# Kernel tuning notes

Measured on AMD Instinct MI355X. Metric: run time of the kernel, lower is better.

Reference implementation:

```python
import jax, jax.numpy as jnp
import numpy as np

BN_EPS = 1e-5

def conv1x1(x, w, b):
    # x: [B,C,H,W], w: [O,C], b: [O] -> [B,O,H,W]
    return jnp.einsum('bchw,oc->bohw', x, w) + b[None, :, None, None]

def maxpool2x2(x):
    B, C, H, W = x.shape
    return x.reshape(B, C, H // 2, 2, W // 2, 2).max(axis=(3, 5))

def setup_inputs() -> dict:
    key = jax.random.key(0)
    ks = jax.random.split(key, 12)
    B, C, Ci, H, W = 8, 256, 128, 64, 64
    s_in = 1.0 / np.sqrt(C)
    s_mid = 1.0 / np.sqrt(Ci)
    return {
        'x': jax.random.normal(ks[0], (B, C, H, W), jnp.float32),
        'y': jax.random.normal(ks[1], (B, C, H, W), jnp.float32),
        'theta_w': jax.random.normal(ks[2], (Ci, C), jnp.float32) * s_in,
        'theta_b': jax.random.normal(ks[3], (Ci,), jnp.float32) * s_in,
        'phi_w': jax.random.normal(ks[4], (Ci, C), jnp.float32) * s_in,
        'phi_b': jax.random.normal(ks[5], (Ci,), jnp.float32) * s_in,
        'g_w': jax.random.normal(ks[6], (Ci, C), jnp.float32) * s_in,
        'g_b': jax.random.normal(ks[7], (Ci,), jnp.float32) * s_in,
        'w_w': jax.random.normal(ks[8], (C, Ci), jnp.float32) * s_mid,
        'w_b': jax.random.normal(ks[9], (C,), jnp.float32) * s_mid,
        'bn_gamma': jax.random.normal(ks[10], (C,), jnp.float32),
        'bn_beta': jax.random.normal(ks[11], (C,), jnp.float32),
    }

def reference(x, y, theta_w, theta_b, phi_w, phi_b, g_w, g_b, w_w, w_b, bn_gamma, bn_beta):
    B, C, H, W = x.shape
    Ci = theta_w.shape[0]
    # Q: [B, N, Ci] from x (no subsample)
    theta_x = conv1x1(x, theta_w, theta_b).reshape(B, Ci, H * W).transpose(0, 2, 1)
    # K: [B, Ci, M] and V: [B, M, Ci] from y (2x2 maxpool subsample)
    phi_x = maxpool2x2(conv1x1(y, phi_w, phi_b)).reshape(B, Ci, -1)
    g_x = maxpool2x2(conv1x1(y, g_w, g_b)).reshape(B, Ci, -1).transpose(0, 2, 1)
    # unscaled dot-product attention, softmax over keys
    f = jnp.einsum('bnc,bcm->bnm', theta_x, phi_x)        # [B, N, M]
    attn = jax.nn.softmax(f, axis=-1)
    out = jnp.einsum('bnm,bmc->bnc', attn, g_x)            # [B, N, Ci]
    out = out.transpose(0, 2, 1).reshape(B, Ci, H, W)
    # W projection (1x1 conv) + BatchNorm (batch statistics, training mode)
    wy = conv1x1(out, w_w, w_b)
    mean = wy.mean(axis=(0, 2, 3))
    var = wy.var(axis=(0, 2, 3))
    wy = (wy - mean[None, :, None, None]) * jax.lax.rsqrt(var[None, :, None, None] + BN_EPS)
    wy = wy * bn_gamma[None, :, None, None] + bn_beta[None, :, None, None]
    return wy + x
```

## Files before the change

kernel.cpp:

```cpp
#include <hip/hip_runtime.h>

#define B_  8
#define C_  256
#define CI_ 128
#define N_  4096
#define M_  1024

typedef unsigned short u16;
typedef _Float16 f16;
typedef __attribute__((ext_vector_type(8))) short short8;
typedef __attribute__((ext_vector_type(8))) _Float16 half8;
typedef __attribute__((ext_vector_type(4))) _Float16 half4;
typedef __attribute__((ext_vector_type(4))) float f32x4;

__device__ __forceinline__ u16 f2bf(float f) {
    unsigned int u = __float_as_uint(f);
    u += 0x7fffu + ((u >> 16) & 1u);
    return (u16)(u >> 16);
}

__global__ __launch_bounds__(256) void prep_w_kernel(
    const float* __restrict__ tw, const float* __restrict__ pw,
    const float* __restrict__ gw, const float* __restrict__ ww,
    f16* __restrict__ out_h)
{
    int t = blockIdx.x * 256 + threadIdx.x;
    int wsel = t >> 12, idx = t & 4095;
    int lane = idx & 63;
    const float* src; int F, Cdim;
    if (wsel == 3)      { src = ww; F = 16; Cdim = 128; }
    else if (wsel == 0) { src = tw; F = 8;  Cdim = 256; }
    else if (wsel == 1) { src = pw; F = 8;  Cdim = 256; }
    else                { src = gw; F = 8;  Cdim = 256; }
    int fk = idx >> 6;
    int ks = fk / F, f = fk - ks * F;
    int o = f * 16 + (lane & 15);
    int c = ks * 32 + (lane >> 4) * 8;
    const float* s = src + (size_t)o * Cdim + c;
    float4 v0 = *(const float4*)s;
    float4 v1 = *(const float4*)(s + 4);
    half8 hv;
    hv[0] = (f16)v0.x; hv[1] = (f16)v0.y; hv[2] = (f16)v0.z; hv[3] = (f16)v0.w;
    hv[4] = (f16)v1.x; hv[5] = (f16)v1.y; hv[6] = (f16)v1.z; hv[7] = (f16)v1.w;
    size_t oo = (size_t)wsel * 32768 + (size_t)idx * 8;
    *(half8*)&out_h[oo] = hv;
}

__global__ __launch_bounds__(256) void qconv_kernel(
    const float* __restrict__ x,
    const f16* __restrict__ Bfh, const float* __restrict__ bias,
    f16* __restrict__ qh_out)
{
    const int tid = threadIdx.x;
    const int wave = tid >> 6, lane = tid & 63;
    const int tx = lane & 15, quad = lane >> 4;
    const int id = blockIdx.x;
    const int ot = (id >> 3) & 1;
    const int p  = (id & 7) | ((id >> 4) << 3);
    const int nb = p & 63;
    const int b  = p >> 6;
    const int nw = nb * 64 + wave * 16;

    f32x4 acc[4];
    #pragma unroll
    for (int i = 0; i < 4; ++i) acc[i] = (f32x4){0.f, 0.f, 0.f, 0.f};

    #pragma unroll
    for (int ks = 0; ks < 8; ++ks) {
        const size_t cbase = ((size_t)b * C_ + ks * 32 + quad * 8) * N_ + nw + tx;
        float a[8];
        #pragma unroll
        for (int j = 0; j < 8; ++j) a[j] = x[cbase + (size_t)j * N_];
        half8 ah;
        #pragma unroll
        for (int j = 0; j < 8; ++j) ah[j] = (f16)a[j];
        #pragma unroll
        for (int fi = 0; fi < 4; ++fi) {
            int f = ot * 4 + fi;
            size_t bo = ((size_t)(ks * 8 + f) * 64 + lane) * 8;
            half8 bh = *(const half8*)&Bfh[bo];
            acc[fi] = __builtin_amdgcn_mfma_f32_16x16x32_f16(ah, bh, acc[fi], 0, 0, 0);
        }
    }

    #pragma unroll
    for (int fi = 0; fi < 4; ++fi) {
        int f = ot * 4 + fi;
        float bv = bias[f * 16 + tx];
        #pragma unroll
        for (int r = 0; r < 4; ++r) {
            size_t addr = ((size_t)(b * N_ + nw + quad * 4 + r)) * CI_ + f * 16 + tx;
            qh_out[addr] = (f16)(acc[fi][r] + bv);
        }
    }
}

__global__ __launch_bounds__(256) void kvconv_kernel(
    const float* __restrict__ y,
    const f16* __restrict__ PfH, const f16* __restrict__ GfH,
    const float* __restrict__ phib, const float* __restrict__ gb,
    f16* __restrict__ khi, u16* __restrict__ vf)
{
    const int tid = threadIdx.x;
    const int w = tid >> 6, lane = tid & 63;
    const int tx = lane & 15, quad = lane >> 4;
    const int id = blockIdx.x;
    const int ot = (id >> 3) & 1;
    const int p  = (id & 7) | ((id >> 4) << 3);
    const int t = p & 31;
    const int b = p >> 5;

    const size_t nA = (size_t)t * 128 + w * 16 + tx;
    const size_t nB = nA + 64;

    f32x4 accP[2][4], accG[2][4];
    #pragma unroll
    for (int i = 0; i < 2; ++i)
        #pragma unroll
        for (int j = 0; j < 4; ++j) {
            accP[i][j] = (f32x4){0.f, 0.f, 0.f, 0.f};
            accG[i][j] = (f32x4){0.f, 0.f, 0.f, 0.f};
        }

    #pragma unroll
    for (int ks = 0; ks < 8; ++ks) {
        const size_t cbase = ((size_t)b * C_ + ks * 32 + quad * 8) * N_;
        float a0[8], a1[8];
        #pragma unroll
        for (int j = 0; j < 8; ++j) {
            a0[j] = y[cbase + (size_t)j * N_ + nA];
            a1[j] = y[cbase + (size_t)j * N_ + nB];
        }
        half8 ah0, ah1;
        #pragma unroll
        for (int j = 0; j < 8; ++j) {
            ah0[j] = (f16)a0[j];
            ah1[j] = (f16)a1[j];
        }
        #pragma unroll
        for (int of = 0; of < 4; ++of) {
            int f = ot * 4 + of;
            size_t bo = ((size_t)(ks * 8 + f) * 64 + lane) * 8;
            half8 ph = *(const half8*)&PfH[bo];
            half8 gh = *(const half8*)&GfH[bo];
            accP[0][of] = __builtin_amdgcn_mfma_f32_16x16x32_f16(ah0, ph, accP[0][of], 0, 0, 0);
            accP[1][of] = __builtin_amdgcn_mfma_f32_16x16x32_f16(ah1, ph, accP[1][of], 0, 0, 0);
            accG[0][of] = __builtin_amdgcn_mfma_f32_16x16x32_f16(ah0, gh, accG[0][of], 0, 0, 0);
            accG[1][of] = __builtin_amdgcn_mfma_f32_16x16x32_f16(ah1, gh, accG[1][of], 0, 0, 0);
        }
    }

    #pragma unroll
    for (int of = 0; of < 4; ++of) {
        int ci = (ot * 4 + of) * 16 + tx;
        float pb = phib[ci], gbv = gb[ci];
        #pragma unroll
        for (int j = 0; j < 2; ++j) {
            float vP = fmaxf(fmaxf(accP[0][of][2 * j], accP[0][of][2 * j + 1]),
                             fmaxf(accP[1][of][2 * j], accP[1][of][2 * j + 1])) + pb;
            float vG = fmaxf(fmaxf(accG[0][of][2 * j], accG[0][of][2 * j + 1]),
                             fmaxf(accG[1][of][2 * j], accG[1][of][2 * j + 1])) + gbv;
            int mm = 8 * w + 2 * quad + j;
            int fragK = (mm >> 4) * 4 + (ci >> 5);
            int laneK = (((ci & 31) >> 3) << 4) + (mm & 15);
            size_t ka = (((size_t)(b * 32 + t) * 8 + fragK) * 64 + laneK) * 8 + (ci & 7);
            khi[ka] = (f16)vP;
            int fragV = ci >> 4;
            size_t va = (((size_t)(b * 32 + t) * 8 + fragV) * 64 + w * 16 + tx) * 8 + (2 * quad + j);
            vf[va] = f2bf(vG);
        }
    }
}

__global__ __launch_bounds__(512) void attn_kernel(
    const f16* __restrict__ Qh, const f16* __restrict__ Kf,
    const u16* __restrict__ Vf, f16* __restrict__ Oh)
{
    __shared__ __align__(16) f16 kh_sh[2][16384];
    __shared__ __align__(16) u16 vf_sh[2][16384];
    __shared__ __align__(16) u16 p_sh[8][16 * 40];

    const int tid = threadIdx.x;
    const int wave = tid >> 6, lane = tid & 63;
    const int tx = lane & 15, quad = lane >> 4;
    const int id = blockIdx.x;
    const int b = id & 7;
    const int q0 = (id >> 3) * 128 + wave * 16;
    const float FM = 48.f;

    half8 qh[4];
    {
        const f16* qp = Qh + ((size_t)b * N_ + q0 + tx) * CI_ + quad * 8;
        #pragma unroll
        for (int ks = 0; ks < 4; ++ks) qh[ks] = *(const half8*)&qp[ks * 32];
    }

    f32x4 acc[8];
    #pragma unroll
    for (int f = 0; f < 8; ++f) acc[f] = (f32x4){0.f, 0.f, 0.f, 0.f};
    float lrun[4] = {0.f, 0.f, 0.f, 0.f};

    const f16* Khb = Kf + (size_t)b * 32 * 4096;
    const u16* Vb  = Vf + (size_t)b * 32 * 4096;
    const int i0 = tid * 8;
    u16* pw_ = p_sh[wave];

    half8 rk[4]; short8 rv[4];
    #pragma unroll
    for (int rp = 0; rp < 4; ++rp) {
        rk[rp] = *(const half8*)&Khb[rp * 4096 + i0];
        rv[rp] = *(const short8*)&Vb[rp * 4096 + i0];
    }

    for (int s = 0; s < 8; ++s) {
        const int cur = s & 1;
        #pragma unroll
        for (int rp = 0; rp < 4; ++rp) {
            *(half8*)&kh_sh[cur][rp * 4096 + i0] = rk[rp];
            *(short8*)&vf_sh[cur][rp * 4096 + i0] = rv[rp];
        }
        if (s + 1 < 8) {
            const size_t base = (size_t)(s + 1) * 16384;
            #pragma unroll
            for (int rp = 0; rp < 4; ++rp) {
                rk[rp] = *(const half8*)&Khb[base + rp * 4096 + i0];
                rv[rp] = *(const short8*)&Vb[base + rp * 4096 + i0];
            }
        }
        asm volatile("s_waitcnt lgkmcnt(0)" ::: "memory");
        __builtin_amdgcn_s_barrier();
        asm volatile("" ::: "memory");

        #pragma unroll
        for (int sub = 0; sub < 4; ++sub) {
            const f16* ksrc = &kh_sh[cur][sub * 4096];
            const u16* vsrc = &vf_sh[cur][sub * 4096];
            half8 bh[8];
            #pragma unroll
            for (int ks = 0; ks < 8; ++ks) bh[ks] = *(const half8*)&ksrc[ks * 512 + lane * 8];
            short8 vb[8];
            #pragma unroll
            for (int f = 0; f < 8; ++f) vb[f] = *(const short8*)&vsrc[f * 512 + lane * 8];

            f32x4 s0 = (f32x4){0.f, 0.f, 0.f, 0.f};
            f32x4 s1 = (f32x4){0.f, 0.f, 0.f, 0.f};
            __builtin_amdgcn_s_setprio(1);
            #pragma unroll
            for (int ks = 0; ks < 4; ++ks) {
                s0 = __builtin_amdgcn_mfma_f32_16x16x32_f16(qh[ks], bh[ks], s0, 0, 0, 0);
                s1 = __builtin_amdgcn_mfma_f32_16x16x32_f16(qh[ks], bh[4 + ks], s1, 0, 0, 0);
            }
            __builtin_amdgcn_s_setprio(0);

            #pragma unroll
            for (int r = 0; r < 4; ++r) {
                float p0 = __expf(s0[r] - FM);
                float p1 = __expf(s1[r] - FM);
                lrun[r] += p0 + p1;
                pw_[(4 * quad + r) * 40 + tx]      = f2bf(p0);
                pw_[(4 * quad + r) * 40 + 16 + tx] = f2bf(p1);
            }
            asm volatile("s_waitcnt lgkmcnt(0)" ::: "memory");
            short8 pf = *(const short8*)&pw_[tx * 40 + quad * 8];

            __builtin_amdgcn_s_setprio(1);
            #pragma unroll
            for (int f = 0; f < 8; ++f)
                acc[f] = __builtin_amdgcn_mfma_f32_16x16x32_bf16(pf, vb[f], acc[f], 0, 0, 0);
            __builtin_amdgcn_s_setprio(0);
        }
    }

    #pragma unroll
    for (int d = 1; d < 16; d <<= 1) {
        #pragma unroll
        for (int r = 0; r < 4; ++r) lrun[r] += __shfl_xor(lrun[r], d);
    }
    float inv[4];
    #pragma unroll
    for (int r = 0; r < 4; ++r) inv[r] = 1.f / lrun[r];
    f16* Ob = Oh + ((size_t)b * N_ + q0) * CI_;
    #pragma unroll
    for (int f = 0; f < 8; ++f) {
        #pragma unroll
        for (int r = 0; r < 4; ++r)
            Ob[(size_t)(4 * quad + r) * CI_ + f * 16 + tx] = (f16)(acc[f][r] * inv[r]);
    }
}

__global__ __launch_bounds__(256) void wconv_mfma_kernel(
    const f16* __restrict__ Bh, const f16* __restrict__ Afh,
    const float* __restrict__ bias, f16* __restrict__ wy,
    float* __restrict__ part)
{
    const int tid = threadIdx.x;
    const int wave = tid >> 6, lane = tid & 63;
    const int tx = lane & 15, quad = lane >> 4;
    const int gnt = blockIdx.x;
    const int b = gnt >> 7;
    const int n0 = (gnt & 127) * 32;
    const int of0 = wave * 4;

    half8 wah[4][4];
    #pragma unroll
    for (int ks = 0; ks < 4; ++ks) {
        #pragma unroll
        for (int ff = 0; ff < 4; ++ff) {
            size_t aa = ((size_t)(ks * 16 + of0 + ff) * 64 + lane) * 8;
            wah[ks][ff] = *(const half8*)&Afh[aa];
        }
    }

    f32x4 acc[4][2];
    #pragma unroll
    for (int i = 0; i < 4; ++i)
        #pragma unroll
        for (int j = 0; j < 2; ++j) acc[i][j] = (f32x4){0.f, 0.f, 0.f, 0.f};

    #pragma unroll
    for (int ks = 0; ks < 4; ++ks) {
        half8 bh[2];
        #pragma unroll
        for (int nf = 0; nf < 2; ++nf) {
            size_t ba = ((size_t)(b * N_ + n0 + nf * 16 + tx)) * CI_ + ks * 32 + quad * 8;
            bh[nf] = *(const half8*)&Bh[ba];
        }
        #pragma unroll
        for (int ff = 0; ff < 4; ++ff)
            #pragma unroll
            for (int nf = 0; nf < 2; ++nf)
                acc[ff][nf] = __builtin_amdgcn_mfma_f32_16x16x32_f16(wah[ks][ff], bh[nf], acc[ff][nf], 0, 0, 0);
    }

    #pragma unroll
    for (int ff = 0; ff < 4; ++ff) {
        int fg = of0 + ff;
        #pragma unroll
        for (int r = 0; r < 4; ++r) {
            int o = fg * 16 + quad * 4 + r;
            float bo = bias[o];
            float ps = 0.f, pss = 0.f;
            #pragma unroll
            for (int nf = 0; nf < 2; ++nf) {
                float v = acc[ff][nf][r] + bo;
                wy[((size_t)b * C_ + o) * N_ + n0 + nf * 16 + tx] = (f16)v;
                ps += v; pss += v * v;
            }
            #pragma unroll
            for (int d = 1; d < 16; d <<= 1) {
                ps  += __shfl_xor(ps, d);
                pss += __shfl_xor(pss, d);
            }
            if (tx == 0) {
                part[(size_t)o * 1024 + gnt]          = ps;
                part[262144 + (size_t)o * 1024 + gnt] = pss;
            }
        }
    }
}

__global__ __launch_bounds__(256) void bn_reduce_kernel(
    const float* __restrict__ part, float* __restrict__ sums)
{
    int w = blockIdx.x * 4 + (threadIdx.x >> 6);
    int lane = threadIdx.x & 63;
    int p = w >> 8, o = w & 255;
    const float* src = part + (size_t)p * 262144 + (size_t)o * 1024;
    float s = 0.f;
    #pragma unroll
    for (int j = 0; j < 16; ++j) s += src[j * 64 + lane];
    #pragma unroll
    for (int d = 1; d < 64; d <<= 1) s += __shfl_xor(s, d);
    if (lane == 0) sums[p * 256 + o] = s;
}

__global__ __launch_bounds__(256) void bn_final_kernel(
    const f16* __restrict__ wy, const float* __restrict__ x,
    const float* __restrict__ gsum, const float* __restrict__ gsumsq,
    const float* __restrict__ gamma, const float* __restrict__ beta,
    float* __restrict__ out)
{
    int idx = blockIdx.x * 256 + threadIdx.x;
    size_t base = (size_t)idx * 4;
    int o = (int)((base >> 12) & 255);
    half4 wv = *(const half4*)&wy[base];
    float4 xv = *(const float4*)&x[base];
    const float invc = 1.f / 32768.f;
    float mean = gsum[o] * invc;
    float var  = gsumsq[o] * invc - mean * mean;
    float sc = gamma[o] * rsqrtf(var + 1e-5f);
    float sh = beta[o] - mean * sc;
    float4 r;
    r.x = (float)wv[0] * sc + sh + xv.x;
    r.y = (float)wv[1] * sc + sh + xv.y;
    r.z = (float)wv[2] * sc + sh + xv.z;
    r.w = (float)wv[3] * sc + sh + xv.w;
    *(float4*)&out[base] = r;
}

extern "C" void kernel_launch(void* const* d_in, const int* in_sizes, int n_in,
                              void* d_out, int out_size, void* d_ws, size_t ws_size,
                              hipStream_t stream) {
    (void)in_sizes; (void)n_in; (void)out_size; (void)ws_size;
    const float* x       = (const float*)d_in[0];
    const float* y       = (const float*)d_in[1];
    const float* theta_w = (const float*)d_in[2];
    const float* theta_b = (const float*)d_in[3];
    const float* phi_w   = (const float*)d_in[4];
    const float* phi_b   = (const float*)d_in[5];
    const float* g_w     = (const float*)d_in[6];
    const float* g_b     = (const float*)d_in[7];
    const float* w_w     = (const float*)d_in[8];
    const float* w_b     = (const float*)d_in[9];
    const float* bn_g    = (const float*)d_in[10];
    const float* bn_b    = (const float*)d_in[11];
    float* out = (float*)d_out;

    float* ws = (float*)d_ws;
    f16*   Qh   = (f16*)(ws);
    f16*   Kf   = (f16*)(ws + 2097152);
    u16*   Vfp  = (u16*)(ws + 2621440);
    f16*   Oh   = (f16*)(ws + 7405568);
    f16*   WY   = (f16*)(ws + 9502720);
    float* PART = ws + 13697024;
    f16*   Wfh  = (f16*)(ws + 14221312);
    float* SUMS = ws + 14286848;

    prep_w_kernel<<<64, 256, 0, stream>>>(theta_w, phi_w, g_w, w_w, Wfh);

    qconv_kernel<<<1024, 256, 0, stream>>>(x, Wfh, theta_b, Qh);
    kvconv_kernel<<<512, 256, 0, stream>>>(
        y, Wfh + 32768, Wfh + 65536, phi_b, g_b, Kf, Vfp);

    attn_kernel<<<256, 512, 0, stream>>>(Qh, Kf, Vfp, Oh);

    wconv_mfma_kernel<<<1024, 256, 0, stream>>>(Oh, Wfh + 98304, w_b, WY, PART);
    bn_reduce_kernel<<<128, 256, 0, stream>>>(PART, SUMS);
    bn_final_kernel<<<8192, 256, 0, stream>>>(WY, x, SUMS, SUMS + 256, bn_g, bn_b, out);
}
```

Baseline: 200.1 us.

## Load K/V fragments directly from global memory instead of LDS staging

Removes the double-buffered shared-memory staging of K and V tiles and the block-wide barrier, so each wave reads its MFMA operand fragments straight from global memory (served by L2/L1) for each of the 32 key chunks. This drops LDS capacity use, which can raise occupancy, and removes the barrier stalls. In exchange, every wave now reads the same K/V data independently, which multiplies cache traffic and exposes global-load latency, since nothing is prefetched ahead.

```diff
diff --git a/kernel.cpp b/kernel.cpp
--- a/kernel.cpp
+++ b/kernel.cpp
@@ -176,8 +176,6 @@
     const f16* __restrict__ Qh, const f16* __restrict__ Kf,
     const u16* __restrict__ Vf, f16* __restrict__ Oh)
 {
-    __shared__ __align__(16) f16 kh_sh[2][16384];
-    __shared__ __align__(16) u16 vf_sh[2][16384];
     __shared__ __align__(16) u16 p_sh[8][16 * 40];
 
     const int tid = threadIdx.x;
@@ -202,73 +200,45 @@
 
     const f16* Khb = Kf + (size_t)b * 32 * 4096;
     const u16* Vb  = Vf + (size_t)b * 32 * 4096;
-    const int i0 = tid * 8;
     u16* pw_ = p_sh[wave];
 
-    half8 rk[4]; short8 rv[4];
-    #pragma unroll
-    for (int rp = 0; rp < 4; ++rp) {
-        rk[rp] = *(const half8*)&Khb[rp * 4096 + i0];
-        rv[rp] = *(const short8*)&Vb[rp * 4096 + i0];
-    }
-
-    for (int s = 0; s < 8; ++s) {
-        const int cur = s & 1;
-        #pragma unroll
-        for (int rp = 0; rp < 4; ++rp) {
-            *(half8*)&kh_sh[cur][rp * 4096 + i0] = rk[rp];
-            *(short8*)&vf_sh[cur][rp * 4096 + i0] = rv[rp];
-        }
-        if (s + 1 < 8) {
-            const size_t base = (size_t)(s + 1) * 16384;
-            #pragma unroll
-            for (int rp = 0; rp < 4; ++rp) {
-                rk[rp] = *(const half8*)&Khb[base + rp * 4096 + i0];
-                rv[rp] = *(const short8*)&Vb[base + rp * 4096 + i0];
-            }
+    for (int ch = 0; ch < 32; ++ch) {
+        const f16* ksrc = Khb + (size_t)ch * 4096;
+        const u16* vsrc = Vb + (size_t)ch * 4096;
+
+        half8 bh[8];
+        #pragma unroll
+        for (int ks = 0; ks < 8; ++ks) bh[ks] = *(const half8*)&ksrc[ks * 512 + lane * 8];
+        short8 vb[8];
+        #pragma unroll
+        for (int f = 0; f < 8; ++f) vb[f] = *(const short8*)&vsrc[f * 512 + lane * 8];
+
+        f32x4 s0 = (f32x4){0.f, 0.f, 0.f, 0.f};
+        f32x4 s1 = (f32x4){0.f, 0.f, 0.f, 0.f};
+        __builtin_amdgcn_s_setprio(1);
+        #pragma unroll
+        for (int ks = 0; ks < 4; ++ks) {
+            s0 = __builtin_amdgcn_mfma_f32_16x16x32_f16(qh[ks], bh[ks], s0, 0, 0, 0);
+            s1 = __builtin_amdgcn_mfma_f32_16x16x32_f16(qh[ks], bh[4 + ks], s1, 0, 0, 0);
+        }
+        __builtin_amdgcn_s_setprio(0);
+
+        #pragma unroll
+        for (int r = 0; r < 4; ++r) {
+            float p0 = __expf(s0[r] - FM);
+            float p1 = __expf(s1[r] - FM);
+            lrun[r] += p0 + p1;
+            pw_[(4 * quad + r) * 40 + tx]      = f2bf(p0);
+            pw_[(4 * quad + r) * 40 + 16 + tx] = f2bf(p1);
         }
         asm volatile("s_waitcnt lgkmcnt(0)" ::: "memory");
-        __builtin_amdgcn_s_barrier();
-        asm volatile("" ::: "memory");
-
-        #pragma unroll
-        for (int sub = 0; sub < 4; ++sub) {
-            const f16* ksrc = &kh_sh[cur][sub * 4096];
-            const u16* vsrc = &vf_sh[cur][sub * 4096];
-            half8 bh[8];
-            #pragma unroll
-            for (int ks = 0; ks < 8; ++ks) bh[ks] = *(const half8*)&ksrc[ks * 512 + lane * 8];
-            short8 vb[8];
-            #pragma unroll
-            for (int f = 0; f < 8; ++f) vb[f] = *(const short8*)&vsrc[f * 512 + lane * 8];
-
-            f32x4 s0 = (f32x4){0.f, 0.f, 0.f, 0.f};
-            f32x4 s1 = (f32x4){0.f, 0.f, 0.f, 0.f};
-            __builtin_amdgcn_s_setprio(1);
-            #pragma unroll
-            for (int ks = 0; ks < 4; ++ks) {
-                s0 = __builtin_amdgcn_mfma_f32_16x16x32_f16(qh[ks], bh[ks], s0, 0, 0, 0);
-                s1 = __builtin_amdgcn_mfma_f32_16x16x32_f16(qh[ks], bh[4 + ks], s1, 0, 0, 0);
-            }
-            __builtin_amdgcn_s_setprio(0);
-
-            #pragma unroll
-            for (int r = 0; r < 4; ++r) {
-                float p0 = __expf(s0[r] - FM);
-                float p1 = __expf(s1[r] - FM);
-                lrun[r] += p0 + p1;
-                pw_[(4 * quad + r) * 40 + tx]      = f2bf(p0);
-                pw_[(4 * quad + r) * 40 + 16 + tx] = f2bf(p1);
-            }
-            asm volatile("s_waitcnt lgkmcnt(0)" ::: "memory");
-            short8 pf = *(const short8*)&pw_[tx * 40 + quad * 8];
-
-            __builtin_amdgcn_s_setprio(1);
-            #pragma unroll
-            for (int f = 0; f < 8; ++f)
-                acc[f] = __builtin_amdgcn_mfma_f32_16x16x32_bf16(pf, vb[f], acc[f], 0, 0, 0);
-            __builtin_amdgcn_s_setprio(0);
-        }
+        short8 pf = *(const short8*)&pw_[tx * 40 + quad * 8];
+
+        __builtin_amdgcn_s_setprio(1);
+        #pragma unroll
+        for (int f = 0; f < 8; ++f)
+            acc[f] = __builtin_amdgcn_mfma_f32_16x16x32_bf16(pf, vb[f], acc[f], 0, 0, 0);
+        __builtin_amdgcn_s_setprio(0);
     }
 
     #pragma unroll
```

Result: slower. 205.8 us (+2.9%).
